# Kernel optimization log

Hardware: AMD Instinct MI355X
Metric: run time of the kernel (lower is better)

Reference implementation:

```python
import jax, jax.numpy as jnp
import numpy as np

B, VN, QN, KN = 64, 100, 64, 64
V_DIM, Q_DIM, KG_DIM = 2048, 768, 300
H_DIM, RANK, GLIMPSE = 1024, 32, 2
HD = H_DIM // RANK  # 32


def setup_inputs() -> dict:
    key = jax.random.key(0)
    ks = jax.random.split(key, 10)
    v = jax.random.normal(ks[0], (B, VN, V_DIM), jnp.float32)
    # zero out last 10 regions so the padding mask path is exercised
    v = v.at[:, VN - 10:, :].set(0.0)
    q = jax.random.normal(ks[1], (B, QN, Q_DIM), jnp.float32)
    kg = jax.random.normal(ks[2], (B, KN, KG_DIM), jnp.float32)
    s = lambda d: 1.0 / np.sqrt(d)
    Wv = jax.random.normal(ks[3], (V_DIM, H_DIM), jnp.float32) * s(V_DIM)
    bv = jnp.zeros((H_DIM,), jnp.float32)
    Wq = jax.random.normal(ks[4], (Q_DIM, H_DIM), jnp.float32) * s(Q_DIM)
    bq = jnp.zeros((H_DIM,), jnp.float32)
    Wkg = jax.random.normal(ks[5], (KG_DIM, H_DIM), jnp.float32) * s(KG_DIM)
    bkg = jnp.zeros((H_DIM,), jnp.float32)
    # core tensor (torch init is normal_(); scaled down so softmax isn't saturated)
    T_g = jax.random.normal(ks[6], (1, RANK, HD, HD, HD, GLIMPSE), jnp.float32) * 0.02
    return {"v": v, "q": q, "kg": kg, "Wv": Wv, "bv": bv, "Wq": Wq, "bq": bq,
            "Wkg": Wkg, "bkg": bkg, "T_g": T_g}


def _tri_logits(v, q, kg, Wv, bv, Wq, bq, Wkg, bkg, T_g):
    b, vn = v.shape[:2]
    qn, kn = q.shape[1], kg.shape[1]
    rank, hd, g = T_g.shape[1], T_g.shape[2], T_g.shape[-1]
    fc = lambda x, W, bb: jax.nn.relu(x @ W + bb)  # FCNet (weight-norm Linear + ReLU), eval: no dropout
    # project to h_dim and split into `rank` contiguous chunks of size hd -> [R,B,N,hd]
    vt = jnp.transpose(fc(v, Wv, bv).reshape(b, vn, rank, hd), (2, 0, 1, 3))
    qt = jnp.transpose(fc(q, Wq, bq).reshape(b, qn, rank, hd), (2, 0, 1, 3))
    kt = jnp.transpose(fc(kg, Wkg, bkg).reshape(b, kn, rank, hd), (2, 0, 1, 3))

    def step(acc, xs):
        vr, qr, kr, Tr = xs  # [B,V,hd],[B,Q,hd],[B,K,hd],[hd,hd,hd,g]
        t = jnp.einsum('bvx,xyzg->bvyzg', vr, Tr)
        t = jnp.einsum('bvyzg,bqy->bvqzg', t, qr)
        t = jnp.einsum('bvqzg,bkz->bvqkg', t, kr)
        return acc + t, None

    init = jnp.zeros((b, vn, qn, kn, g), v.dtype)
    logits, _ = jax.lax.scan(step, init, (vt, qt, kt, T_g[0]))
    return logits  # [B,V,Q,K,glimpse]


def reference(v, q, kg, Wv, bv, Wq, bq, Wkg, bkg, T_g):
    b, vn = v.shape[:2]
    qn, kn = q.shape[1], kg.shape[1]
    g = T_g.shape[-1]
    logits = _tri_logits(v, q, kg, Wv, bv, Wq, bq, Wkg, bkg, T_g)
    # mask padded image regions (all-zero feature rows)
    mask = jnp.sum(jnp.abs(v), axis=2) == 0  # [B,V]
    logits = jnp.where(mask[:, :, None, None, None], -jnp.inf, logits)
    # softmax over the flattened V*Q*K axis, per glimpse
    p = jax.nn.softmax(logits.reshape(b, vn * qn * kn, g), axis=1)
    return p.reshape(b, vn, qn, kn, g), logits
```

## Files before the change

### kernel.cpp

```cpp
#include <hip/hip_runtime.h>
#include <cstdint>
#include <math.h>

#define MASK_VAL (-1e30f)

#define Bb   64
#define VN   100
#define QN   64
#define KN   64
#define VD   2048
#define QD   768
#define KGD  300
#define KGP  320
#define HH   1024
#define RR   32
#define HDm  32
#define GG   2
#define NBV  (Bb*VN)
#define LOGN ((size_t)NBV*QN*KN*GG)

typedef _Float16 half_t;
typedef _Float16 f16x8 __attribute__((ext_vector_type(8)));
typedef _Float16 f16x4 __attribute__((ext_vector_type(4)));
typedef float    f32x4 __attribute__((ext_vector_type(4)));

#define MFMA_F16(a,b,c) __builtin_amdgcn_mfma_f32_16x16x32_f16(a,b,c,0,0,0)

#define PN0 13107200
#define PN1 3145728
#define PN2 1310720
#define PN3 2097152
#define PN4 786432
#define PN5 327680
#define PN6 2097152
#define PTOT (PN0+PN1+PN2+PN3+PN4+PN5+PN6)

__device__ inline void fm_decode(long d, int KB, int& row, int& k) {
  int blk = (int)(d >> 9);
  int lc = (int)((d >> 7) & 3), lr = (int)((d >> 3) & 15), h = (int)(d & 7);
  row = (blk / KB) * 16 + lr;
  k   = (blk % KB) * 32 + lc*8 + h;
}

__global__ __launch_bounds__(256) void preproc_kernel(const float* __restrict__ v,
                                                      const float* __restrict__ q,
                                                      const float* __restrict__ kg,
                                                      const float* __restrict__ Wv,
                                                      const float* __restrict__ Wq,
                                                      const float* __restrict__ Wkg,
                                                      const float* __restrict__ Tg,
                                                      half_t* __restrict__ v16,
                                                      half_t* __restrict__ q16,
                                                      half_t* __restrict__ k16,
                                                      half_t* __restrict__ Wvt,
                                                      half_t* __restrict__ Wqt,
                                                      half_t* __restrict__ Wkt,
                                                      half_t* __restrict__ Tpp)
{
  long idx = (long)blockIdx.x*256 + threadIdx.x;
  if (idx >= PTOT) return;
  int row, k;
  if (idx < PN0) { fm_decode(idx, 64, row, k); v16[idx] = (half_t)v[(size_t)row*VD + k]; return; }
  idx -= PN0;
  if (idx < PN1) { fm_decode(idx, 24, row, k); q16[idx] = (half_t)q[(size_t)row*QD + k]; return; }
  idx -= PN1;
  if (idx < PN2) {
    fm_decode(idx, 10, row, k);
    k16[idx] = (half_t)((k < KGD) ? kg[(size_t)row*KGD + k] : 0.f);
    return;
  }
  idx -= PN2;
  if (idx < PN3) { fm_decode(idx, 64, row, k); Wvt[idx] = (half_t)Wv[(size_t)k*HH + row]; return; }
  idx -= PN3;
  if (idx < PN4) { fm_decode(idx, 24, row, k); Wqt[idx] = (half_t)Wq[(size_t)k*HH + row]; return; }
  idx -= PN4;
  if (idx < PN5) {
    fm_decode(idx, 10, row, k);
    Wkt[idx] = (half_t)((k < KGD) ? Wkg[(size_t)k*HH + row] : 0.f);
    return;
  }
  idx -= PN5;
  {
    int r = (int)(idx >> 16), rem = (int)(idx & 65535);
    int cp = rem >> 5, x = rem & 31;
    int y = cp & 31, zg = cp >> 5;
    Tpp[idx + (size_t)0] = (half_t)Tg[((size_t)(r*32 + x) << 11) + y*64 + zg];
  }
}

__global__ __launch_bounds__(256) void mask_kernel(const float* __restrict__ v,
                                                   float* __restrict__ maskv)
{
  int row = blockIdx.x;
  int tid = threadIdx.x;
  const float* src = v + (size_t)row * VD;
  float s = 0.f;
  for (int i = tid; i < VD/4; i += 256) {
    float4 x = *(const float4*)&src[i*4];
    s += fabsf(x.x)+fabsf(x.y)+fabsf(x.z)+fabsf(x.w);
  }
#pragma unroll
  for (int off=32; off; off>>=1) s += __shfl_down(s, off);
  __shared__ float red[4];
  if ((tid & 63) == 0) red[tid>>6] = s;
  __syncthreads();
  if (tid == 0) maskv[row] = ((red[0]+red[1]+red[2]+red[3]) == 0.f) ? 1.f : 0.f;
}

__global__ __launch_bounds__(256) void proj_mfma_kernel(const half_t* __restrict__ A0,
                                                        const half_t* __restrict__ A1,
                                                        const half_t* __restrict__ A2,
                                                        const half_t* __restrict__ W0,
                                                        const half_t* __restrict__ W1,
                                                        const half_t* __restrict__ W2,
                                                        const float* __restrict__ b0p,
                                                        const float* __restrict__ b1p,
                                                        const float* __restrict__ b2p,
                                                        half_t* __restrict__ H0,
                                                        half_t* __restrict__ H1,
                                                        half_t* __restrict__ H2)
{
  int z = blockIdx.z;
  int Mb = (z == 0) ? 100 : 64;
  if ((int)blockIdx.x >= Mb) return;
  const half_t* A  = (z==0) ? A0 : (z==1) ? A1 : A2;
  const half_t* Wt = (z==0) ? W0 : (z==1) ? W1 : W2;
  const float* bias = (z==0) ? b0p : (z==1) ? b1p : b2p;
  half_t* H = (z==0) ? H0 : (z==1) ? H1 : H2;
  int KB = (z==0) ? 64 : (z==1) ? 24 : 10;

  int w = threadIdx.x >> 6, lane = threadIdx.x & 63;
  int mtile = blockIdx.x*4 + w;
  int n0 = blockIdx.y*64;
  int lr = lane & 15, lc = lane >> 4;
  f32x4 acc[4];
#pragma unroll
  for (int nt=0;nt<4;nt++) acc[nt] = (f32x4)(0.f);
  const half_t* abase = A + ((size_t)mtile*KB)*512 + lane*8;
  const half_t* wbase = Wt + ((size_t)(blockIdx.y*4)*KB)*512 + lane*8;
  for (int kb = 0; kb < KB; kb++) {
    f16x8 a = *(const f16x8*)(abase + (size_t)kb*512);
#pragma unroll
    for (int nt = 0; nt < 4; nt++) {
      f16x8 b = *(const f16x8*)(wbase + ((size_t)nt*KB + kb)*512);
      acc[nt] = MFMA_F16(a, b, acc[nt]);
    }
  }
  int m0 = mtile*16;
#pragma unroll
  for (int nt = 0; nt < 4; nt++) {
    float bb = bias[n0 + nt*16 + lr];
#pragma unroll
    for (int j = 0; j < 4; j++) {
      float vv = fmaxf(acc[nt][j] + bb, 0.f);
      H[(size_t)(m0 + lc*4 + j)*HH + n0 + nt*16 + lr] = (half_t)vv;
    }
  }
}

__global__ __launch_bounds__(256) void stageA_mfma_kernel(const half_t* __restrict__ hv,
                                                          const half_t* __restrict__ Tpp,
                                                          half_t* __restrict__ u, int r0)
{
  __shared__ half_t tile[4][16][256];
  int rc = blockIdx.z; int r = r0 + rc;
  int w = threadIdx.x >> 6, lane = threadIdx.x & 63;
  int m0 = blockIdx.x*64 + w*16;
  int n0 = blockIdx.y*256;
  int lr = lane & 15, lc = lane >> 4;
  f16x8 bH = *(const f16x8*)(hv + (size_t)(m0 + lr)*HH + r*HDm + lc*8);
  const half_t* ta = Tpp + ((size_t)r << 16) + (size_t)n0*32 + lr*32 + lc*8;
  half_t* myt = &tile[w][0][0];
#pragma unroll
  for (int t = 0; t < 16; t++) {
    f16x8 aT = *(const f16x8*)(ta + t*512);
    f32x4 d = MFMA_F16(aT, bH, (f32x4)(0.f));
    f16x4 pk;
    pk[0] = (half_t)d[0]; pk[1] = (half_t)d[1];
    pk[2] = (half_t)d[2]; pk[3] = (half_t)d[3];
    int col4 = (t*4 + lc) ^ (lr & 14);
    *(f16x4*)(myt + lr*256 + col4*4) = pk;
  }
  half_t* ub = u + ((size_t)rc*NBV + m0)*2048 + n0;
  int hl = lane >> 5;
  int cc = lane & 31;
#pragma unroll
  for (int i = 0; i < 8; i++) {
    int rrow = i*2 + hl;
    int pc4 = (cc*2) ^ (rrow & 14);
    f16x8 val = *(const f16x8*)(myt + rrow*256 + pc4*4);
    *(f16x8*)(ub + (size_t)rrow*2048 + cc*8) = val;
  }
}

__global__ __launch_bounds__(256,2) void triBC_mfma_kernel(const half_t* __restrict__ hq,
                                                           const half_t* __restrict__ hk,
                                                           const half_t* __restrict__ u,
                                                           const float* __restrict__ maskv,
                                                           uint32_t* __restrict__ logits16,
                                                           float* __restrict__ pm,
                                                           float* __restrict__ ps,
                                                           int r0, int RC, int isFirst, int isLast)
{
  __shared__ __align__(16) half_t qtf[2][2048];
  __shared__ __align__(16) half_t ktf[2][2048];
  __shared__ uint32_t wlds[4][2048];
  int tid = threadIdx.x;
  int w = tid >> 6, lane = tid & 63;
  uint32_t* wme = wlds[w];
  int vt = blockIdx.x, b = blockIdx.y;
  int bv = b*VN + vt*4 + w;
  int lr = lane & 15, lc = lane >> 4;

  int bvb = b*VN + vt*4;
  float mk0 = maskv[bvb+0], mk1 = maskv[bvb+1], mk2 = maskv[bvb+2], mk3 = maskv[bvb+3];
  bool myMasked = ((w==0?mk0 : w==1?mk1 : w==2?mk2 : mk3) != 0.f);
  bool allMasked = (mk0!=0.f) && (mk1!=0.f) && (mk2!=0.f) && (mk3!=0.f);
  if (allMasked) {
    if (isLast) {
      union { uint32_t u32; half_t h[2]; } pk;
      pk.h[0] = (half_t)MASK_VAL; pk.h[1] = (half_t)MASK_VAL;
      uint32_t* lb16 = logits16 + (size_t)bv*QN*KN;
#pragma unroll
      for (int mt=0;mt<4;mt++)
#pragma unroll
        for (int nt=0;nt<4;nt++)
#pragma unroll
          for (int j=0;j<4;j++)
            lb16[(size_t)(mt*16 + lc*4 + j)*KN + nt*16 + lr] = pk.u32;
      if (lane == 0) {
        pm[(size_t)bv*GG+0] = MASK_VAL; ps[(size_t)bv*GG+0] = 4096.f;
        pm[(size_t)bv*GG+1] = MASK_VAL; ps[(size_t)bv*GG+1] = 4096.f;
      }
    }
    return;
  }

  f32x4 acc[2][4][4];
#pragma unroll
  for (int g=0;g<2;g++)
#pragma unroll
    for (int mt=0;mt<4;mt++)
#pragma unroll
      for (int nt=0;nt<4;nt++) acc[g][mt][nt] = (f32x4)(0.f);

  int srow = tid >> 2, sch = tid & 3;
  const half_t* qsrc = hq + (size_t)(b*QN + srow)*HH + sch*8;
  const half_t* ksrc = hk + (size_t)(b*KN + srow)*HH + sch*8;
  int sdst = (srow>>4)*512 + ((srow&15) + sch*16)*8;
  const half_t* ulane = u + (size_t)bv*2048 + lr*HDm + lc*8;

  *(f16x8*)&qtf[0][sdst] = *(const f16x8*)(qsrc + r0*HDm);
  *(f16x8*)&ktf[0][sdst] = *(const f16x8*)(ksrc + r0*HDm);
  int rp1 = (RC > 1) ? 1 : 0;
  f16x8 qhold = *(const f16x8*)(qsrc + (r0+rp1)*HDm);
  f16x8 khold = *(const f16x8*)(ksrc + (r0+rp1)*HDm);
  f16x8 ub[4];
  if (!myMasked) {
#pragma unroll
    for (int nt=0;nt<4;nt++) ub[nt] = *(const f16x8*)(ulane + nt*512);
  }
  asm volatile("s_waitcnt lgkmcnt(0)" ::: "memory");
  __builtin_amdgcn_s_barrier();

  for (int rc = 0; rc < RC; rc++) {
    int bp = rc & 1;
    int rn1 = (rc+1 < RC) ? rc+1 : RC-1;
    int rn2 = (rc+2 < RC) ? rc+2 : RC-1;
    *(f16x8*)&qtf[bp^1][sdst] = qhold;
    *(f16x8*)&ktf[bp^1][sdst] = khold;
    qhold = *(const f16x8*)(qsrc + (r0+rn2)*HDm);
    khold = *(const f16x8*)(ksrc + (r0+rn2)*HDm);
    if (!myMasked) {
      f16x8 qa[4], bk[4];
#pragma unroll
      for (int mt=0;mt<4;mt++) qa[mt] = *(const f16x8*)&qtf[bp][mt*512 + lane*8];
#pragma unroll
      for (int nt=0;nt<4;nt++) bk[nt] = *(const f16x8*)&ktf[bp][nt*512 + lane*8];
      f16x8 ubN[4];
#pragma unroll
      for (int nt=0;nt<4;nt++)
        ubN[nt] = *(const f16x8*)(ulane + (size_t)rn1*NBV*2048 + nt*512);
#pragma unroll
      for (int t=0;t<4;t++) {
#pragma unroll
        for (int mt=0;mt<4;mt++) {
          f32x4 d = MFMA_F16(ub[t], qa[mt], (f32x4)(0.f));
          union { uint32_t u32; half_t h[2]; } p0, p1;
          p0.h[0] = (half_t)d[0]; p0.h[1] = (half_t)d[2];
          p1.h[0] = (half_t)d[1]; p1.h[1] = (half_t)d[3];
          wme[(t*8 + 0*4 + mt)*64 + lr*4 + lc] = p0.u32;
          wme[(t*8 + 1*4 + mt)*64 + lr*4 + lc] = p1.u32;
        }
      }
#pragma unroll
      for (int g=0;g<2;g++) {
        f16x8 am[4];
#pragma unroll
        for (int mt=0;mt<4;mt++)
          am[mt] = *(const f16x8*)&wme[(lc*8 + g*4 + mt)*64 + lr*4];
#pragma unroll
        for (int mt=0;mt<4;mt++)
#pragma unroll
          for (int nt=0;nt<4;nt++)
            acc[g][mt][nt] = MFMA_F16(am[mt], bk[nt], acc[g][mt][nt]);
      }
#pragma unroll
      for (int nt=0;nt<4;nt++) ub[nt] = ubN[nt];
    }
    asm volatile("s_waitcnt lgkmcnt(0)" ::: "memory");
    __builtin_amdgcn_s_barrier();
  }

  uint32_t* lb16 = logits16 + (size_t)bv*QN*KN;
  if (myMasked) {
    if (isLast) {
      union { uint32_t u32; half_t h[2]; } pk;
      pk.h[0] = (half_t)MASK_VAL; pk.h[1] = (half_t)MASK_VAL;
#pragma unroll
      for (int mt=0;mt<4;mt++)
#pragma unroll
        for (int nt=0;nt<4;nt++)
#pragma unroll
          for (int j=0;j<4;j++)
            lb16[(size_t)(mt*16 + lc*4 + j)*KN + nt*16 + lr] = pk.u32;
      if (lane == 0) {
        pm[(size_t)bv*GG+0] = MASK_VAL; ps[(size_t)bv*GG+0] = 4096.f;
        pm[(size_t)bv*GG+1] = MASK_VAL; ps[(size_t)bv*GG+1] = 4096.f;
      }
    }
    return;
  }
#pragma unroll
  for (int mt=0;mt<4;mt++)
#pragma unroll
    for (int nt=0;nt<4;nt++)
#pragma unroll
      for (int j=0;j<4;j++) {
        size_t off = (size_t)(mt*16 + lc*4 + j)*KN + nt*16 + lr;
        float g0 = acc[0][mt][nt][j], g1 = acc[1][mt][nt][j];
        if (!isFirst) {
          union { uint32_t u32; half_t h[2]; } pv;
          pv.u32 = lb16[off];
          g0 += (float)pv.h[0]; g1 += (float)pv.h[1];
        }
        union { uint32_t u32; half_t h[2]; } pk;
        pk.h[0] = (half_t)g0; pk.h[1] = (half_t)g1;
        lb16[off] = pk.u32;
        acc[0][mt][nt][j] = g0; acc[1][mt][nt][j] = g1;
      }
  if (isLast) {
#pragma unroll
    for (int g=0; g<2; g++) {
      float mloc = acc[g][0][0][0];
#pragma unroll
      for (int mt=0;mt<4;mt++)
#pragma unroll
        for (int nt=0;nt<4;nt++)
#pragma unroll
          for (int j=0;j<4;j++) mloc = fmaxf(mloc, acc[g][mt][nt][j]);
      float sloc = 0.f;
#pragma unroll
      for (int mt=0;mt<4;mt++)
#pragma unroll
        for (int nt=0;nt<4;nt++)
#pragma unroll
          for (int j=0;j<4;j++) sloc += __expf(acc[g][mt][nt][j] - mloc);
#pragma unroll
      for (int off2=1; off2<64; off2<<=1) {
        float m2 = __shfl_xor(mloc, off2);
        float s2 = __shfl_xor(sloc, off2);
        float mn = fmaxf(mloc, m2);
        sloc = sloc*__expf(mloc-mn) + s2*__expf(m2-mn);
        mloc = mn;
      }
      if (lane == 0) { pm[(size_t)bv*GG + g] = mloc; ps[(size_t)bv*GG + g] = sloc; }
    }
  }
}

__global__ __launch_bounds__(64) void combine_kernel(const float* __restrict__ pm,
                                                     const float* __restrict__ ps,
                                                     float* __restrict__ Mg, float* __restrict__ Sg)
{
  int bg = blockIdx.x; int b = bg >> 1, g = bg & 1;
  int lane = threadIdx.x;
  float m = pm[((size_t)b*VN + lane)*GG + g];
  float s = ps[((size_t)b*VN + lane)*GG + g];
  if (lane + 64 < VN) {
    float m2 = pm[((size_t)b*VN + lane + 64)*GG + g];
    float s2 = ps[((size_t)b*VN + lane + 64)*GG + g];
    float mn = fmaxf(m, m2);
    s = s*__expf(m-mn) + s2*__expf(m2-mn); m = mn;
  }
#pragma unroll
  for (int off=1; off<64; off<<=1) {
    float m2 = __shfl_xor(m, off);
    float s2 = __shfl_xor(s, off);
    float mn = fmaxf(m, m2);
    s = s*__expf(m-mn) + s2*__expf(m2-mn);
    m = mn;
  }
  if (lane == 0) { Mg[b*GG+g] = m; Sg[b*GG+g] = s; }
}

__global__ __launch_bounds__(256) void pwrite16_kernel(const uint32_t* __restrict__ lg,
                                                       const float* __restrict__ Mg,
                                                       const float* __restrict__ Sg,
                                                       float* __restrict__ p)
{
  const size_t PER_B = (size_t)VN*QN*KN;
  const size_t n2 = LOGN/4;
  size_t stride = (size_t)gridDim.x * 256;
  for (size_t t = (size_t)blockIdx.x*256 + threadIdx.x; t < n2; t += stride) {
    size_t i0 = t*2;
    int b = (int)(i0 / PER_B);
    float M0 = Mg[b*2], M1 = Mg[b*2+1];
    float iS0 = 1.f/Sg[b*2], iS1 = 1.f/Sg[b*2+1];
    union { uint2 v; half_t h[4]; } x;
    x.v = *(const uint2*)&lg[i0];
    float4 o;
    o.x = __expf((float)x.h[0] - M0)*iS0;
    o.y = __expf((float)x.h[1] - M1)*iS1;
    o.z = __expf((float)x.h[2] - M0)*iS0;
    o.w = __expf((float)x.h[3] - M1)*iS1;
    *(float4*)&p[i0*2] = o;
  }
}

extern "C" void kernel_launch(void* const* d_in, const int* in_sizes, int n_in,
                              void* d_out, int out_size, void* d_ws, size_t ws_size,
                              hipStream_t stream)
{
  const float* v   = (const float*)d_in[0];
  const float* q   = (const float*)d_in[1];
  const float* kg  = (const float*)d_in[2];
  const float* Wv  = (const float*)d_in[3];
  const float* bv  = (const float*)d_in[4];
  const float* Wq  = (const float*)d_in[5];
  const float* bq  = (const float*)d_in[6];
  const float* Wkg = (const float*)d_in[7];
  const float* bkg = (const float*)d_in[8];
  const float* Tg  = (const float*)d_in[9];
  float* p_out  = (float*)d_out;
  uint32_t* logits16 = (uint32_t*)(p_out + LOGN);

  char* ws = (char*)d_ws;
  size_t off = 0;
  auto alloc = [&](size_t bytes) -> char* {
    char* ptr = ws + off;
    off = (off + bytes + 255) & ~(size_t)255;
    return ptr;
  };
  half_t* h_v16 = (half_t*)alloc((size_t)NBV*HH*2);
  half_t* h_q16 = (half_t*)alloc((size_t)Bb*QN*HH*2);
  half_t* h_k16 = (half_t*)alloc((size_t)Bb*KN*HH*2);
  half_t* v16   = (half_t*)alloc((size_t)NBV*VD*2);
  half_t* q16   = (half_t*)alloc((size_t)Bb*QN*QD*2);
  half_t* k16   = (half_t*)alloc((size_t)Bb*KN*KGP*2);
  half_t* Wvt   = (half_t*)alloc((size_t)HH*VD*2);
  half_t* Wqt   = (half_t*)alloc((size_t)HH*QD*2);
  half_t* Wkt   = (half_t*)alloc((size_t)HH*KGP*2);
  half_t* Tpp   = (half_t*)alloc((size_t)32*65536*2);
  float* maskv  = (float*)alloc((size_t)NBV*4);
  float* pm     = (float*)alloc((size_t)NBV*GG*4);
  float* ps     = (float*)alloc((size_t)NBV*GG*4);
  float* Mg     = (float*)alloc(128*4);
  float* Sg     = (float*)alloc(128*4);
  size_t WS_FIXED = off;
  const size_t USZB = (size_t)NBV*2048*2;

  int RC; half_t* u;
  if      (WS_FIXED + 32*USZB <= ws_size) { RC = 32; u = (half_t*)(ws + off); }
  else if (WS_FIXED + 16*USZB <= ws_size) { RC = 16; u = (half_t*)(ws + off); }
  else if (WS_FIXED +  8*USZB <= ws_size) { RC =  8; u = (half_t*)(ws + off); }
  else { RC = 8; u = (half_t*)p_out; }

  preproc_kernel<<<(unsigned)((PTOT + 255)/256),256,0,stream>>>(v, q, kg, Wv, Wq, Wkg, Tg,
                                                                v16, q16, k16, Wvt, Wqt, Wkt, Tpp);
  mask_kernel<<<NBV,256,0,stream>>>(v, maskv);

  proj_mfma_kernel<<<dim3(100,16,3),256,0,stream>>>(v16, q16, k16, Wvt, Wqt, Wkt,
                                                    bv, bq, bkg, h_v16, h_q16, h_k16);

  for (int r0 = 0; r0 < RR; r0 += RC) {
    stageA_mfma_kernel<<<dim3(100,8,RC),256,0,stream>>>(h_v16, Tpp, u, r0);
    triBC_mfma_kernel<<<dim3(25,Bb),256,0,stream>>>(h_q16, h_k16, u, maskv, logits16, pm, ps,
                                                    r0, RC, (r0==0)?1:0, (r0+RC>=RR)?1:0);
  }
  combine_kernel<<<128,64,0,stream>>>(pm, ps, Mg, Sg);
  pwrite16_kernel<<<2048,256,0,stream>>>(logits16, Mg, Sg, p_out);
}
```

Measured before the change: 671.2 us.

## Chunk stage-A/triBC over batch instead of rank to keep intermediate cache-resident

The intermediate u buffer was split by rank, and when the workspace was small the logits were re-read and accumulated across several passes. It is now split into 4 batch chunks of 1600 rows, and each pass handles all 32 ranks. Each u chunk is about 210 MB, which removes the read-modify-write of the fp16 logits across rank chunks and makes every triBC launch run the full rank loop. The cost is fewer blocks per triBC launch (25x16 instead of 25x64), so parallelism per launch drops.

Result: faster. 641.1 us (-4.5%).

```diff
diff --git a/kernel.cpp b/kernel.cpp
--- a/kernel.cpp
+++ b/kernel.cpp
@@ -19,6 +19,10 @@
 #define NBV  (Bb*VN)
 #define LOGN ((size_t)NBV*QN*KN*GG)
 
+#define NCHUNK 4
+#define BVC    1600
+#define BCH    16
+
 typedef _Float16 half_t;
 typedef _Float16 f16x8 __attribute__((ext_vector_type(8)));
 typedef _Float16 f16x4 __attribute__((ext_vector_type(4)));
@@ -160,15 +164,15 @@
 
 __global__ __launch_bounds__(256) void stageA_mfma_kernel(const half_t* __restrict__ hv,
                                                           const half_t* __restrict__ Tpp,
-                                                          half_t* __restrict__ u, int r0)
+                                                          half_t* __restrict__ u, int bv0)
 {
   __shared__ half_t tile[4][16][256];
-  int rc = blockIdx.z; int r = r0 + rc;
+  int rc = blockIdx.z; int r = rc;
   int w = threadIdx.x >> 6, lane = threadIdx.x & 63;
   int m0 = blockIdx.x*64 + w*16;
   int n0 = blockIdx.y*256;
   int lr = lane & 15, lc = lane >> 4;
-  f16x8 bH = *(const f16x8*)(hv + (size_t)(m0 + lr)*HH + r*HDm + lc*8);
+  f16x8 bH = *(const f16x8*)(hv + (size_t)(bv0 + m0 + lr)*HH + r*HDm + lc*8);
   const half_t* ta = Tpp + ((size_t)r << 16) + (size_t)n0*32 + lr*32 + lc*8;
   half_t* myt = &tile[w][0][0];
 #pragma unroll
@@ -181,7 +185,7 @@
     int col4 = (t*4 + lc) ^ (lr & 14);
     *(f16x4*)(myt + lr*256 + col4*4) = pk;
   }
-  half_t* ub = u + ((size_t)rc*NBV + m0)*2048 + n0;
+  half_t* ub = u + ((size_t)rc*BVC + m0)*2048 + n0;
   int hl = lane >> 5;
   int cc = lane & 31;
 #pragma unroll
@@ -200,7 +204,7 @@
                                                            uint32_t* __restrict__ logits16,
                                                            float* __restrict__ pm,
                                                            float* __restrict__ ps,
-                                                           int r0, int RC, int isFirst, int isLast)
+                                                           int b0)
 {
   __shared__ __align__(16) half_t qtf[2][2048];
   __shared__ __align__(16) half_t ktf[2][2048];
@@ -208,8 +212,9 @@
   int tid = threadIdx.x;
   int w = tid >> 6, lane = tid & 63;
   uint32_t* wme = wlds[w];
-  int vt = blockIdx.x, b = blockIdx.y;
+  int vt = blockIdx.x, b = b0 + blockIdx.y;
   int bv = b*VN + vt*4 + w;
+  int bvloc = (int)blockIdx.y*VN + vt*4 + w;
   int lr = lane & 15, lc = lane >> 4;
 
   int bvb = b*VN + vt*4;
@@ -217,21 +222,19 @@
   bool myMasked = ((w==0?mk0 : w==1?mk1 : w==2?mk2 : mk3) != 0.f);
   bool allMasked = (mk0!=0.f) && (mk1!=0.f) && (mk2!=0.f) && (mk3!=0.f);
   if (allMasked) {
-    if (isLast) {
-      union { uint32_t u32; half_t h[2]; } pk;
-      pk.h[0] = (half_t)MASK_VAL; pk.h[1] = (half_t)MASK_VAL;
-      uint32_t* lb16 = logits16 + (size_t)bv*QN*KN;
-#pragma unroll
-      for (int mt=0;mt<4;mt++)
-#pragma unroll
-        for (int nt=0;nt<4;nt++)
-#pragma unroll
-          for (int j=0;j<4;j++)
-            lb16[(size_t)(mt*16 + lc*4 + j)*KN + nt*16 + lr] = pk.u32;
-      if (lane == 0) {
-        pm[(size_t)bv*GG+0] = MASK_VAL; ps[(size_t)bv*GG+0] = 4096.f;
-        pm[(size_t)bv*GG+1] = MASK_VAL; ps[(size_t)bv*GG+1] = 4096.f;
-      }
+    union { uint32_t u32; half_t h[2]; } pk;
+    pk.h[0] = (half_t)MASK_VAL; pk.h[1] = (half_t)MASK_VAL;
+    uint32_t* lb16 = logits16 + (size_t)bv*QN*KN;
+#pragma unroll
+    for (int mt=0;mt<4;mt++)
+#pragma unroll
+      for (int nt=0;nt<4;nt++)
+#pragma unroll
+        for (int j=0;j<4;j++)
+          lb16[(size_t)(mt*16 + lc*4 + j)*KN + nt*16 + lr] = pk.u32;
+    if (lane == 0) {
+      pm[(size_t)bv*GG+0] = MASK_VAL; ps[(size_t)bv*GG+0] = 4096.f;
+      pm[(size_t)bv*GG+1] = MASK_VAL; ps[(size_t)bv*GG+1] = 4096.f;
     }
     return;
   }
@@ -248,13 +251,12 @@
   const half_t* qsrc = hq + (size_t)(b*QN + srow)*HH + sch*8;
   const half_t* ksrc = hk + (size_t)(b*KN + srow)*HH + sch*8;
   int sdst = (srow>>4)*512 + ((srow&15) + sch*16)*8;
-  const half_t* ulane = u + (size_t)bv*2048 + lr*HDm + lc*8;
-
-  *(f16x8*)&qtf[0][sdst] = *(const f16x8*)(qsrc + r0*HDm);
-  *(f16x8*)&ktf[0][sdst] = *(const f16x8*)(ksrc + r0*HDm);
-  int rp1 = (RC > 1) ? 1 : 0;
-  f16x8 qhold = *(const f16x8*)(qsrc + (r0+rp1)*HDm);
-  f16x8 khold = *(const f16x8*)(ksrc + (r0+rp1)*HDm);
+  const half_t* ulane = u + (size_t)bvloc*2048 + lr*HDm + lc*8;
+
+  *(f16x8*)&qtf[0][sdst] = *(const f16x8*)(qsrc);
+  *(f16x8*)&ktf[0][sdst] = *(const f16x8*)(ksrc);
+  f16x8 qhold = *(const f16x8*)(qsrc + HDm);
+  f16x8 khold = *(const f16x8*)(ksrc + HDm);
   f16x8 ub[4];
   if (!myMasked) {
 #pragma unroll
@@ -263,14 +265,14 @@
   asm volatile("s_waitcnt lgkmcnt(0)" ::: "memory");
   __builtin_amdgcn_s_barrier();
 
-  for (int rc = 0; rc < RC; rc++) {
+  for (int rc = 0; rc < RR; rc++) {
     int bp = rc & 1;
-    int rn1 = (rc+1 < RC) ? rc+1 : RC-1;
-    int rn2 = (rc+2 < RC) ? rc+2 : RC-1;
+    int rn1 = (rc+1 < RR) ? rc+1 : RR-1;
+    int rn2 = (rc+2 < RR) ? rc+2 : RR-1;
     *(f16x8*)&qtf[bp^1][sdst] = qhold;
     *(f16x8*)&ktf[bp^1][sdst] = khold;
-    qhold = *(const f16x8*)(qsrc + (r0+rn2)*HDm);
-    khold = *(const f16x8*)(ksrc + (r0+rn2)*HDm);
+    qhold = *(const f16x8*)(qsrc + rn2*HDm);
+    khold = *(const f16x8*)(ksrc + rn2*HDm);
     if (!myMasked) {
       f16x8 qa[4], bk[4];
 #pragma unroll
@@ -280,7 +282,7 @@
       f16x8 ubN[4];
 #pragma unroll
       for (int nt=0;nt<4;nt++)
-        ubN[nt] = *(const f16x8*)(ulane + (size_t)rn1*NBV*2048 + nt*512);
+        ubN[nt] = *(const f16x8*)(ulane + (size_t)rn1*BVC*2048 + nt*512);
 #pragma unroll
       for (int t=0;t<4;t++) {
 #pragma unroll
@@ -314,20 +316,18 @@
 
   uint32_t* lb16 = logits16 + (size_t)bv*QN*KN;
   if (myMasked) {
-    if (isLast) {
-      union { uint32_t u32; half_t h[2]; } pk;
-      pk.h[0] = (half_t)MASK_VAL; pk.h[1] = (half_t)MASK_VAL;
-#pragma unroll
-      for (int mt=0;mt<4;mt++)
-#pragma unroll
-        for (int nt=0;nt<4;nt++)
-#pragma unroll
-          for (int j=0;j<4;j++)
-            lb16[(size_t)(mt*16 + lc*4 + j)*KN + nt*16 + lr] = pk.u32;
-      if (lane == 0) {
-        pm[(size_t)bv*GG+0] = MASK_VAL; ps[(size_t)bv*GG+0] = 4096.f;
-        pm[(size_t)bv*GG+1] = MASK_VAL; ps[(size_t)bv*GG+1] = 4096.f;
-      }
+    union { uint32_t u32; half_t h[2]; } pk;
+    pk.h[0] = (half_t)MASK_VAL; pk.h[1] = (half_t)MASK_VAL;
+#pragma unroll
+    for (int mt=0;mt<4;mt++)
+#pragma unroll
+      for (int nt=0;nt<4;nt++)
+#pragma unroll
+        for (int j=0;j<4;j++)
+          lb16[(size_t)(mt*16 + lc*4 + j)*KN + nt*16 + lr] = pk.u32;
+    if (lane == 0) {
+      pm[(size_t)bv*GG+0] = MASK_VAL; ps[(size_t)bv*GG+0] = 4096.f;
+      pm[(size_t)bv*GG+1] = MASK_VAL; ps[(size_t)bv*GG+1] = 4096.f;
     }
     return;
   }
@@ -339,43 +339,35 @@
       for (int j=0;j<4;j++) {
         size_t off = (size_t)(mt*16 + lc*4 + j)*KN + nt*16 + lr;
         float g0 = acc[0][mt][nt][j], g1 = acc[1][mt][nt][j];
-        if (!isFirst) {
-          union { uint32_t u32; half_t h[2]; } pv;
-          pv.u32 = lb16[off];
-          g0 += (float)pv.h[0]; g1 += (float)pv.h[1];
-        }
         union { uint32_t u32; half_t h[2]; } pk;
         pk.h[0] = (half_t)g0; pk.h[1] = (half_t)g1;
         lb16[off] = pk.u32;
-        acc[0][mt][nt][j] = g0; acc[1][mt][nt][j] = g1;
       }
-  if (isLast) {
-#pragma unroll
-    for (int g=0; g<2; g++) {
-      float mloc = acc[g][0][0][0];
-#pragma unroll
-      for (int mt=0;mt<4;mt++)
-#pragma unroll
-        for (int nt=0;nt<4;nt++)
-#pragma unroll
-          for (int j=0;j<4;j++) mloc = fmaxf(mloc, acc[g][mt][nt][j]);
-      float sloc = 0.f;
-#pragma unroll
-      for (int mt=0;mt<4;mt++)
-#pragma unroll
-        for (int nt=0;nt<4;nt++)
-#pragma unroll
-          for (int j=0;j<4;j++) sloc += __expf(acc[g][mt][nt][j] - mloc);
-#pragma unroll
-      for (int off2=1; off2<64; off2<<=1) {
-        float m2 = __shfl_xor(mloc, off2);
-        float s2 = __shfl_xor(sloc, off2);
-        float mn = fmaxf(mloc, m2);
-        sloc = sloc*__expf(mloc-mn) + s2*__expf(m2-mn);
-        mloc = mn;
-      }
-      if (lane == 0) { pm[(size_t)bv*GG + g] = mloc; ps[(size_t)bv*GG + g] = sloc; }
-    }
+#pragma unroll
+  for (int g=0; g<2; g++) {
+    float mloc = acc[g][0][0][0];
+#pragma unroll
+    for (int mt=0;mt<4;mt++)
+#pragma unroll
+      for (int nt=0;nt<4;nt++)
+#pragma unroll
+        for (int j=0;j<4;j++) mloc = fmaxf(mloc, acc[g][mt][nt][j]);
+    float sloc = 0.f;
+#pragma unroll
+    for (int mt=0;mt<4;mt++)
+#pragma unroll
+      for (int nt=0;nt<4;nt++)
+#pragma unroll
+        for (int j=0;j<4;j++) sloc += __expf(acc[g][mt][nt][j] - mloc);
+#pragma unroll
+    for (int off2=1; off2<64; off2<<=1) {
+      float m2 = __shfl_xor(mloc, off2);
+      float s2 = __shfl_xor(sloc, off2);
+      float mn = fmaxf(mloc, m2);
+      sloc = sloc*__expf(mloc-mn) + s2*__expf(m2-mn);
+      mloc = mn;
+    }
+    if (lane == 0) { pm[(size_t)bv*GG + g] = mloc; ps[(size_t)bv*GG + g] = sloc; }
   }
 }
 
@@ -468,13 +460,11 @@
   float* Mg     = (float*)alloc(128*4);
   float* Sg     = (float*)alloc(128*4);
   size_t WS_FIXED = off;
-  const size_t USZB = (size_t)NBV*2048*2;
-
-  int RC; half_t* u;
-  if      (WS_FIXED + 32*USZB <= ws_size) { RC = 32; u = (half_t*)(ws + off); }
-  else if (WS_FIXED + 16*USZB <= ws_size) { RC = 16; u = (half_t*)(ws + off); }
-  else if (WS_FIXED +  8*USZB <= ws_size) { RC =  8; u = (half_t*)(ws + off); }
-  else { RC = 8; u = (half_t*)p_out; }
+  const size_t UCHUNKB = (size_t)RR*BVC*2048*2;
+
+  half_t* u;
+  if (WS_FIXED + UCHUNKB <= ws_size) u = (half_t*)(ws + off);
+  else u = (half_t*)p_out;
 
   preproc_kernel<<<(unsigned)((PTOT + 255)/256),256,0,stream>>>(v, q, kg, Wv, Wq, Wkg, Tg,
                                                                 v16, q16, k16, Wvt, Wqt, Wkt, Tpp);
@@ -483,10 +473,10 @@
   proj_mfma_kernel<<<dim3(100,16,3),256,0,stream>>>(v16, q16, k16, Wvt, Wqt, Wkt,
                                                     bv, bq, bkg, h_v16, h_q16, h_k16);
 
-  for (int r0 = 0; r0 < RR; r0 += RC) {
-    stageA_mfma_kernel<<<dim3(100,8,RC),256,0,stream>>>(h_v16, Tpp, u, r0);
-    triBC_mfma_kernel<<<dim3(25,Bb),256,0,stream>>>(h_q16, h_k16, u, maskv, logits16, pm, ps,
-                                                    r0, RC, (r0==0)?1:0, (r0+RC>=RR)?1:0);
+  for (int c = 0; c < NCHUNK; c++) {
+    stageA_mfma_kernel<<<dim3(BVC/64,8,RR),256,0,stream>>>(h_v16, Tpp, u, c*BVC);
+    triBC_mfma_kernel<<<dim3(25,BCH),256,0,stream>>>(h_q16, h_k16, u, maskv,
+                                                     logits16, pm, ps, c*BCH);
   }
   combine_kernel<<<128,64,0,stream>>>(pm, ps, Mg, Sg);
   pwrite16_kernel<<<2048,256,0,stream>>>(logits16, Mg, Sg, p_out);
```
